# Kernel optimization log

Measured on AMD Instinct MI355X. Metric: run time of the kernel, lower is better.

The kernel has to match this reference:

```python
import jax, jax.numpy as jnp
import numpy as np

B, D, K, E = 4096, 2048, 512, 8  # tokens, model dim, kept SVD rank, experts


def setup_inputs() -> dict:
    key = jax.random.key(0)
    ks = jax.random.split(key, 7)
    x = jax.random.normal(ks[0], (B, D), dtype=jnp.float32)
    # frozen base weight (stands in for pretrained_weight)
    W = jax.random.normal(ks[1], (D, D), dtype=jnp.float32) / np.sqrt(D)
    # frozen truncated SVD factors: U_k (D,K) left vecs, V_k (K,D) as sliced in the torch code
    U_k = jnp.linalg.qr(jax.random.normal(ks[2], (D, K), dtype=jnp.float32))[0]
    V_k = jnp.linalg.qr(jax.random.normal(ks[3], (D, K), dtype=jnp.float32))[0].T
    lambda_k = jax.random.normal(ks[4], (E, K), dtype=jnp.float32) * 0.02
    v = jnp.zeros((D,), dtype=jnp.float32)
    router_W1 = jax.random.normal(ks[5], (K, 1), dtype=jnp.float32)
    router_W2 = jax.random.normal(ks[6], (1, E), dtype=jnp.float32)
    return {"x": x, "W": W, "U_k": U_k, "V_k": V_k, "lambda_k": lambda_k,
            "v": v, "router_W1": router_W1, "router_W2": router_W2}


def reference(x, W, U_k, V_k, lambda_k, v, router_W1, router_W2):
    # routing: x @ U_k -> rank-1 router -> softmax over experts
    routing = x @ U_k                                   # (B,K)
    g = jax.nn.softmax((routing @ router_W1) @ router_W2, axis=-1)  # (B,E)
    # per-expert low-rank delta weight, materialized as in the original
    delta_W = jnp.einsum('dk,ek,kn->edn', U_k, lambda_k, V_k)       # (E,D,D)
    W_tot = W[None] + delta_W                           # (E,D,D)
    # F.linear semantics: out = x @ W_tot^T per expert
    expert_out = jnp.einsum('bd,end->ben', x, W_tot)    # (B,E,D)
    out = jnp.einsum('ben,be->bn', expert_out, g)       # gated combine
    return out * (1.0 + v)
```

## Files before the change

### kernel.cpp

```cpp
#include <hip/hip_runtime.h>
#include <hip/hip_bf16.h>
#include <cstdint>

#define B_TOK 4096
#define DDIM  2048
#define KR    512
#define NE    8

using f32x4  = __attribute__((ext_vector_type(4))) float;
using short8 = __attribute__((ext_vector_type(8))) short;
using u16 = unsigned short;

__device__ inline u16 f2bf(float f) {
    union { float f; uint32_t u; } x; x.f = f;
    uint32_t u = x.u;
    return (u16)((u + 0x7fffu + ((u >> 16) & 1u)) >> 16);
}
__device__ inline float bf2f(u16 h) {
    union { uint32_t u; float f; } x; x.u = ((uint32_t)h) << 16;
    return x.f;
}

__device__ inline void gload_lds16(const u16* g, u16* l) {
    __builtin_amdgcn_global_load_lds(
        (const __attribute__((address_space(1))) void*)g,
        (__attribute__((address_space(3))) void*)l, 16, 0, 0);
}

template<int COLS4, int SRC_LD, int DST_LD>
__device__ inline void cvt_region(const float* __restrict__ src,
                                  u16* __restrict__ dst, int i) {
    int r = i / COLS4, c = i - r * COLS4;
    float4 val = *((const float4*)(src + (size_t)r * SRC_LD) + c);
    ushort4 o;
    o.x = f2bf(val.x); o.y = f2bf(val.y); o.z = f2bf(val.z); o.w = f2bf(val.w);
    *(ushort4*)(dst + (size_t)r * DST_LD + c * 4) = o;
}

__global__ __launch_bounds__(256)
void prep_all(const float* __restrict__ x, const float* __restrict__ U,
              const float* __restrict__ V, const float* __restrict__ W1,
              u16* __restrict__ Aaug, u16* __restrict__ Vb) {
    constexpr int NB_COPY = 1024;
    constexpr int N_X = 4096 * 512;
    constexpr int N_V = 512 * 512;
    constexpr int N_Z = 63 * 512;
    constexpr int N_TOT = N_X + N_V + N_Z;
    int b = blockIdx.x;
    if (b < NB_COPY) {
        for (int i = b * 256 + threadIdx.x; i < N_TOT; i += NB_COPY * 256) {
            if (i < N_X)            cvt_region<512, 2048, 2560>(x, Aaug, i);
            else if (i < N_X + N_V) cvt_region<512, 2048, 2048>(V, Vb, i - N_X);
            else {
                int z = i - (N_X + N_V);
                ushort4 zz; zz.x = 0; zz.y = 0; zz.z = 0; zz.w = 0;
                *(ushort4*)(Vb + (size_t)513 * 2048 + (size_t)z * 4) = zz;
            }
        }
    } else {
        int wrow = (b - NB_COPY) * 4 + (threadIdx.x >> 6);
        int lane = threadIdx.x & 63;
        const float* row = U + (size_t)wrow * KR;
        float s = 0.f;
        #pragma unroll
        for (int k = 0; k < KR; k += 64) s += row[k + lane] * W1[k + lane];
        #pragma unroll
        for (int o = 32; o > 0; o >>= 1) s += __shfl_down(s, o);
        if (lane == 0) Vb[(size_t)512 * 2048 + wrow] = f2bf(s);
    }
}

__global__ __launch_bounds__(256)
void router3(const u16* __restrict__ tb, const float* __restrict__ W2,
             const float* __restrict__ lam, u16* __restrict__ Am) {
    const int row = blockIdx.x * 8 + (threadIdx.x >> 5);
    const int lr = threadIdx.x & 31;
    const u16* tr = tb + (size_t)row * 576;
    float s = bf2f(tr[512]);

    float g[NE]; float mx = -1e30f;
    #pragma unroll
    for (int e = 0; e < NE; e++) { g[e] = s * W2[e]; mx = fmaxf(mx, g[e]); }
    float den = 0.f;
    #pragma unroll
    for (int e = 0; e < NE; e++) { g[e] = expf(g[e] - mx); den += g[e]; }
    float inv = 1.0f / den;

    #pragma unroll
    for (int h = 0; h < 2; h++) {
        int k = (lr + h * 32) * 8;
        short8 tv = *(const short8*)(tr + k);
        short8 ov;
        #pragma unroll
        for (int j = 0; j < 8; j++) {
            float mu = 0.f;
            #pragma unroll
            for (int e = 0; e < NE; e++) mu += g[e] * lam[e * KR + k + j];
            ov[j] = (short)f2bf(mu * inv * bf2f((u16)tv[j]));
        }
        *(short8*)(Am + (size_t)row * 2560 + 2048 + k) = ov;
    }
}

template<int BM, int BN, int WGM, int WGN, int NCOMP, bool OUT_BF16>
__global__ __launch_bounds__(256, 2)
void gemm_db(const u16* __restrict__ A, const u16* __restrict__ Bm,
             void* __restrict__ Cv,
             const float* __restrict__ Wsrc, const float* __restrict__ Usrc,
             u16* __restrict__ BigB,
             int N, int Kc, int lda, int ldb, int nbx) {
    constexpr int MF = BM / (WGM * 16);
    constexpr int NF = BN / (WGN * 16);
    constexpr int ISSA = BM / 32;
    constexpr int ISSB = BN / 32;
    __shared__ u16 sA[2 * BM * 64];
    __shared__ u16 sB[2 * BN * 64];

    if (blockIdx.x >= NCOMP) {
        constexpr int N_W = 2048 * 512;
        constexpr int N_U = 2048 * 128;
        int cb = blockIdx.x - NCOMP;
        for (int i = cb * 256 + threadIdx.x; i < N_W + N_U; i += 256 * 256) {
            if (i < N_W) cvt_region<512, 2048, 2560>(Wsrc, BigB, i);
            else         cvt_region<128, 512, 2560>(Usrc, BigB + 2048, i - N_W);
        }
        return;
    }

    const int tid = threadIdx.x;
    const int wid = tid >> 6, lane = tid & 63;
    const int l15 = lane & 15, l4 = lane >> 4;
    const int wm = wid / WGN, wn = wid % WGN;

    const int id = ((int)blockIdx.x & 7) * (NCOMP >> 3) + ((int)blockIdx.x >> 3);
    const int row0 = (id / nbx) * BM;
    const int col0 = (id % nbx) * BN;

    const int srow = tid >> 3;
    const int scol = ((tid & 7) ^ (srow & 7)) << 3;
    const u16* gA = A + (size_t)(row0 + srow) * lda + scol;
    const u16* gB = Bm + (size_t)(col0 + srow) * ldb + scol;

    f32x4 acc[MF][NF] = {};
    const int nt = Kc >> 6;

    #pragma unroll
    for (int i = 0; i < ISSA; i++)
        gload_lds16(gA + (size_t)i * 32 * lda, sA + i * 2048 + wid * 512);
    #pragma unroll
    for (int i = 0; i < ISSB; i++)
        gload_lds16(gB + (size_t)i * 32 * ldb, sB + i * 2048 + wid * 512);
    __syncthreads();

    for (int t = 0; t < nt; ++t) {
        const int cur = t & 1;
        if (t + 1 < nt) {
            const int nxt = cur ^ 1;
            const u16* gAk = gA + (size_t)(t + 1) * 64;
            const u16* gBk = gB + (size_t)(t + 1) * 64;
            #pragma unroll
            for (int i = 0; i < ISSA; i++)
                gload_lds16(gAk + (size_t)i * 32 * lda,
                            sA + nxt * BM * 64 + i * 2048 + wid * 512);
            #pragma unroll
            for (int i = 0; i < ISSB; i++)
                gload_lds16(gBk + (size_t)i * 32 * ldb,
                            sB + nxt * BN * 64 + i * 2048 + wid * 512);
        }
        const u16* a0 = sA + cur * BM * 64;
        const u16* b0 = sB + cur * BN * 64;
        #pragma unroll
        for (int kc = 0; kc < 8; kc += 4) {
            short8 af[MF], bv[NF];
            #pragma unroll
            for (int mf = 0; mf < MF; mf++) {
                int row = wm * MF * 16 + mf * 16 + l15;
                int ch = (kc + l4) ^ (row & 7);
                af[mf] = *(const short8*)(a0 + row * 64 + ch * 8);
            }
            #pragma unroll
            for (int nf = 0; nf < NF; nf++) {
                int row = wn * NF * 16 + nf * 16 + l15;
                int ch = (kc + l4) ^ (row & 7);
                bv[nf] = *(const short8*)(b0 + row * 64 + ch * 8);
            }
            #pragma unroll
            for (int mf = 0; mf < MF; mf++)
                #pragma unroll
                for (int nf = 0; nf < NF; nf++)
                    acc[mf][nf] = __builtin_amdgcn_mfma_f32_16x16x32_bf16(
                        af[mf], bv[nf], acc[mf][nf], 0, 0, 0);
        }
        __syncthreads();
    }

    #pragma unroll
    for (int nf = 0; nf < NF; nf++) {
        int col = col0 + wn * NF * 16 + nf * 16 + l15;
        #pragma unroll
        for (int mf = 0; mf < MF; mf++) {
            int row = row0 + wm * MF * 16 + mf * 16 + l4 * 4;
            #pragma unroll
            for (int r2 = 0; r2 < 4; r2++) {
                float val = acc[mf][nf][r2];
                if constexpr (OUT_BF16)
                    ((u16*)Cv)[(size_t)(row + r2) * N + col] = f2bf(val);
                else
                    ((float*)Cv)[(size_t)(row + r2) * N + col] = val;
            }
        }
    }
}

template<bool HAS_V>
__global__ __launch_bounds__(512, 1)
void gemm_ring(const u16* __restrict__ A, const u16* __restrict__ Bm,
               float* __restrict__ C, const float* __restrict__ v,
               int N, int Kc, int lda, int ldb) {
    constexpr int BM = 256, BN = 128, WGN = 2;
    constexpr int MF = 4, NF = 4;
    constexpr int SLOT = (BM + BN) * 64;
    constexpr int ROWS = 64;
    constexpr int ISSA = 4, ISSB = 2;
    __shared__ u16 lds[3 * SLOT];

    const int tid = threadIdx.x;
    const int wid = tid >> 6, lane = tid & 63;
    const int l15 = lane & 15, l4 = lane >> 4;
    const int wm = wid / WGN, wn = wid % WGN;

    const int xcd = blockIdx.x & 7;
    const int j = blockIdx.x >> 3;
    const int row0 = ((xcd >> 1) * 4 + (j >> 3)) * BM;
    const int col0 = ((xcd & 1) * 8 + (j & 7)) * BN;

    const int srow = tid >> 3;
    const int scol = ((tid & 7) ^ (srow & 7)) << 3;
    const u16* gA = A + (size_t)(row0 + srow) * lda + scol;
    const u16* gB = Bm + (size_t)(col0 + srow) * ldb + scol;

    int aoff[2][MF], boff[2][NF];
    #pragma unroll
    for (int kc = 0; kc < 2; kc++) {
        #pragma unroll
        for (int mf = 0; mf < MF; mf++) {
            int row = wm * MF * 16 + mf * 16 + l15;
            aoff[kc][mf] = row * 64 + (((kc * 4) + l4) ^ (row & 7)) * 8;
        }
        #pragma unroll
        for (int nf = 0; nf < NF; nf++) {
            int row = wn * NF * 16 + nf * 16 + l15;
            boff[kc][nf] = BM * 64 + row * 64 + (((kc * 4) + l4) ^ (row & 7)) * 8;
        }
    }

    f32x4 acc[MF][NF] = {};
    const int nt = Kc >> 6;

    #pragma unroll
    for (int p = 0; p < 2; p++) {
        const u16* gAt = gA + p * 64;
        const u16* gBt = gB + p * 64;
        u16* sl = lds + p * SLOT;
        #pragma unroll
        for (int i = 0; i < ISSA; i++)
            gload_lds16(gAt + (size_t)i * ROWS * lda,
                        sl + i * ROWS * 64 + wid * 512);
        #pragma unroll
        for (int i = 0; i < ISSB; i++)
            gload_lds16(gBt + (size_t)i * ROWS * ldb,
                        sl + BM * 64 + i * ROWS * 64 + wid * 512);
    }
    asm volatile("s_waitcnt vmcnt(6)" ::: "memory");
    __builtin_amdgcn_s_barrier();
    asm volatile("" ::: "memory");

    int sc = 0, sp = 2;
    for (int t = 0; t < nt; ++t) {
        if (t + 2 < nt) {
            const u16* gAt = gA + (size_t)(t + 2) * 64;
            const u16* gBt = gB + (size_t)(t + 2) * 64;
            u16* sl = lds + sp * SLOT;
            #pragma unroll
            for (int i = 0; i < ISSA; i++)
                gload_lds16(gAt + (size_t)i * ROWS * lda,
                            sl + i * ROWS * 64 + wid * 512);
            #pragma unroll
            for (int i = 0; i < ISSB; i++)
                gload_lds16(gBt + (size_t)i * ROWS * ldb,
                            sl + BM * 64 + i * ROWS * 64 + wid * 512);
        }
        const u16* s0 = lds + sc * SLOT;
        __builtin_amdgcn_s_setprio(1);
        #pragma unroll
        for (int kc = 0; kc < 2; kc++) {
            short8 af[MF], bv[NF];
            #pragma unroll
            for (int mf = 0; mf < MF; mf++)
                af[mf] = *(const short8*)(s0 + aoff[kc][mf]);
            #pragma unroll
            for (int nf = 0; nf < NF; nf++)
                bv[nf] = *(const short8*)(s0 + boff[kc][nf]);
            #pragma unroll
            for (int mf = 0; mf < MF; mf++)
                #pragma unroll
                for (int nf = 0; nf < NF; nf++)
                    acc[mf][nf] = __builtin_amdgcn_mfma_f32_16x16x32_bf16(
                        af[mf], bv[nf], acc[mf][nf], 0, 0, 0);
        }
        __builtin_amdgcn_s_setprio(0);

        const int rem = nt - 1 - t;
        if (rem == 0) break;
        if (rem >= 2) asm volatile("s_waitcnt vmcnt(6)" ::: "memory");
        else          asm volatile("s_waitcnt vmcnt(0)" ::: "memory");
        __builtin_amdgcn_s_barrier();
        asm volatile("" ::: "memory");
        sc = (sc == 2) ? 0 : sc + 1;
        sp = (sp == 2) ? 0 : sp + 1;
    }

    #pragma unroll
    for (int nf = 0; nf < NF; nf++) {
        int col = col0 + wn * NF * 16 + nf * 16 + l15;
        float sc2 = HAS_V ? (1.0f + v[col]) : 1.0f;
        #pragma unroll
        for (int mf = 0; mf < MF; mf++) {
            int row = row0 + wm * MF * 16 + mf * 16 + l4 * 4;
            #pragma unroll
            for (int r2 = 0; r2 < 4; r2++)
                C[(size_t)(row + r2) * N + col] = acc[mf][nf][r2] * sc2;
        }
    }
}

extern "C" void kernel_launch(void* const* d_in, const int* in_sizes, int n_in,
                              void* d_out, int out_size, void* d_ws, size_t ws_size,
                              hipStream_t stream) {
    const float* x   = (const float*)d_in[0];
    const float* W   = (const float*)d_in[1];
    const float* U   = (const float*)d_in[2];
    const float* V   = (const float*)d_in[3];
    const float* lam = (const float*)d_in[4];
    const float* v   = (const float*)d_in[5];
    const float* W1  = (const float*)d_in[6];
    const float* W2  = (const float*)d_in[7];
    float* out = (float*)d_out;

    char* ws = (char*)d_ws;
    u16* Aaug  = (u16*)ws;
    u16* BigB  = (u16*)(ws + 20971520);
    u16* Vb    = (u16*)(ws + 31457280);
    u16* tmatb = (u16*)(ws + 33816576);

    prep_all<<<1536, 256, 0, stream>>>(x, U, V, W1, Aaug, Vb);

    gemm_db<128, 64, 4, 1, 288, true><<<544, 256, 0, stream>>>(
        Aaug, Vb, tmatb, W, U, BigB, 576, 2048, 2560, 2048, 9);

    router3<<<512, 256, 0, stream>>>(tmatb, W2, lam, Aaug);

    gemm_ring<true><<<256, 512, 0, stream>>>(
        Aaug, BigB, out, v, 2048, 2560, 2560, 2560);
}
```

Before: 91.63 us.

## Read fp32 x directly in first GEMM and move x conversion into its side blocks

The first GEMM now stages fp32 x tiles into LDS with a swizzled layout and converts them to bf16 in registers before the MFMA, so it no longer waits on a separate prep pass that converted x. The x-to-bf16 conversion for the final GEMM's A operand moves into the extra copy blocks of the first GEMM, running alongside the W and U conversion, and the prep kernel shrinks to only V, zero padding and the router vector. This shortens the critical path ahead of the first GEMM, at the cost of twice the LDS and global traffic for the A tile, extra conversion ALU work in the inner loop, and fewer copy blocks (224) now handling more data.

After: 97.56 us. 6.5% more time.

```diff
diff --git a/kernel.cpp b/kernel.cpp
--- a/kernel.cpp
+++ b/kernel.cpp
@@ -19,6 +19,10 @@
 __device__ inline float bf2f(u16 h) {
     union { uint32_t u; float f; } x; x.u = ((uint32_t)h) << 16;
     return x.f;
+}
+__device__ inline short bfs(float f) {
+    __hip_bfloat16 h = __float2bfloat16(f);
+    return *reinterpret_cast<short*>(&h);
 }
 
 __device__ inline void gload_lds16(const u16* g, u16* l) {
@@ -38,21 +42,17 @@
 }
 
 __global__ __launch_bounds__(256)
-void prep_all(const float* __restrict__ x, const float* __restrict__ U,
-              const float* __restrict__ V, const float* __restrict__ W1,
-              u16* __restrict__ Aaug, u16* __restrict__ Vb) {
-    constexpr int NB_COPY = 1024;
-    constexpr int N_X = 4096 * 512;
+void prep_small(const float* __restrict__ U, const float* __restrict__ V,
+                const float* __restrict__ W1, u16* __restrict__ Vb) {
+    constexpr int NB_COPY = 64;
     constexpr int N_V = 512 * 512;
     constexpr int N_Z = 63 * 512;
-    constexpr int N_TOT = N_X + N_V + N_Z;
     int b = blockIdx.x;
     if (b < NB_COPY) {
-        for (int i = b * 256 + threadIdx.x; i < N_TOT; i += NB_COPY * 256) {
-            if (i < N_X)            cvt_region<512, 2048, 2560>(x, Aaug, i);
-            else if (i < N_X + N_V) cvt_region<512, 2048, 2048>(V, Vb, i - N_X);
+        for (int i = b * 256 + threadIdx.x; i < N_V + N_Z; i += NB_COPY * 256) {
+            if (i < N_V) cvt_region<512, 2048, 2048>(V, Vb, i);
             else {
-                int z = i - (N_X + N_V);
+                int z = i - N_V;
                 ushort4 zz; zz.x = 0; zz.y = 0; zz.z = 0; zz.w = 0;
                 *(ushort4*)(Vb + (size_t)513 * 2048 + (size_t)z * 4) = zz;
             }
@@ -102,27 +102,27 @@
     }
 }
 
-template<int BM, int BN, int WGM, int WGN, int NCOMP, bool OUT_BF16>
+template<int NCOMP>
 __global__ __launch_bounds__(256, 2)
-void gemm_db(const u16* __restrict__ A, const u16* __restrict__ Bm,
-             void* __restrict__ Cv,
-             const float* __restrict__ Wsrc, const float* __restrict__ Usrc,
-             u16* __restrict__ BigB,
-             int N, int Kc, int lda, int ldb, int nbx) {
-    constexpr int MF = BM / (WGM * 16);
-    constexpr int NF = BN / (WGN * 16);
-    constexpr int ISSA = BM / 32;
-    constexpr int ISSB = BN / 32;
-    __shared__ u16 sA[2 * BM * 64];
-    __shared__ u16 sB[2 * BN * 64];
+void gemm1_f32(const float* __restrict__ xf, const u16* __restrict__ Bm,
+               u16* __restrict__ Cb,
+               const float* __restrict__ Wsrc, const float* __restrict__ Usrc,
+               u16* __restrict__ BigB, u16* __restrict__ Aaug,
+               int N, int Kc, int nbx) {
+    constexpr int BM = 128, BN = 64;
+    constexpr int MF = 2, NF = 4;
+    __shared__ float sAf[2 * BM * 64];
+    __shared__ u16   sB [2 * BN * 64];
 
     if (blockIdx.x >= NCOMP) {
+        constexpr int N_X = 4096 * 512;
         constexpr int N_W = 2048 * 512;
         constexpr int N_U = 2048 * 128;
         int cb = blockIdx.x - NCOMP;
-        for (int i = cb * 256 + threadIdx.x; i < N_W + N_U; i += 256 * 256) {
-            if (i < N_W) cvt_region<512, 2048, 2560>(Wsrc, BigB, i);
-            else         cvt_region<128, 512, 2560>(Usrc, BigB + 2048, i - N_W);
+        for (int i = cb * 256 + threadIdx.x; i < N_X + N_W + N_U; i += 224 * 256) {
+            if (i < N_X)            cvt_region<512, 2048, 2560>(xf, Aaug, i);
+            else if (i < N_X + N_W) cvt_region<512, 2048, 2560>(Wsrc, BigB, i - N_X);
+            else                    cvt_region<128, 512, 2560>(Usrc, BigB + 2048, i - N_X - N_W);
         }
         return;
     }
@@ -130,57 +130,68 @@
     const int tid = threadIdx.x;
     const int wid = tid >> 6, lane = tid & 63;
     const int l15 = lane & 15, l4 = lane >> 4;
-    const int wm = wid / WGN, wn = wid % WGN;
+    const int wm = wid;
 
     const int id = ((int)blockIdx.x & 7) * (NCOMP >> 3) + ((int)blockIdx.x >> 3);
     const int row0 = (id / nbx) * BM;
     const int col0 = (id % nbx) * BN;
 
-    const int srow = tid >> 3;
-    const int scol = ((tid & 7) ^ (srow & 7)) << 3;
-    const u16* gA = A + (size_t)(row0 + srow) * lda + scol;
-    const u16* gB = Bm + (size_t)(col0 + srow) * ldb + scol;
+    const int sra = tid >> 4;
+    const int sca = ((tid & 15) ^ sra) << 2;
+    const float* gA = xf + (size_t)(row0 + sra) * 2048 + sca;
+    const int srb = tid >> 3;
+    const int scb = ((tid & 7) ^ (srb & 7)) << 3;
+    const u16* gB = Bm + (size_t)(col0 + srb) * 2048 + scb;
+
+    auto stageA = [&](int kt, int buf) {
+        #pragma unroll
+        for (int i = 0; i < 8; i++)
+            gload_lds16((const u16*)(gA + (size_t)i * 16 * 2048 + kt),
+                        (u16*)(sAf + buf * 8192 + i * 1024 + wid * 256));
+    };
+    auto stageB = [&](int kt, int buf) {
+        #pragma unroll
+        for (int i = 0; i < 2; i++)
+            gload_lds16(gB + (size_t)i * 32 * 2048 + kt,
+                        sB + buf * 4096 + i * 2048 + wid * 512);
+    };
 
     f32x4 acc[MF][NF] = {};
     const int nt = Kc >> 6;
 
-    #pragma unroll
-    for (int i = 0; i < ISSA; i++)
-        gload_lds16(gA + (size_t)i * 32 * lda, sA + i * 2048 + wid * 512);
-    #pragma unroll
-    for (int i = 0; i < ISSB; i++)
-        gload_lds16(gB + (size_t)i * 32 * ldb, sB + i * 2048 + wid * 512);
+    stageB(0, 0);
+    stageA(0, 0);
     __syncthreads();
 
     for (int t = 0; t < nt; ++t) {
         const int cur = t & 1;
         if (t + 1 < nt) {
-            const int nxt = cur ^ 1;
-            const u16* gAk = gA + (size_t)(t + 1) * 64;
-            const u16* gBk = gB + (size_t)(t + 1) * 64;
-            #pragma unroll
-            for (int i = 0; i < ISSA; i++)
-                gload_lds16(gAk + (size_t)i * 32 * lda,
-                            sA + nxt * BM * 64 + i * 2048 + wid * 512);
-            #pragma unroll
-            for (int i = 0; i < ISSB; i++)
-                gload_lds16(gBk + (size_t)i * 32 * ldb,
-                            sB + nxt * BN * 64 + i * 2048 + wid * 512);
-        }
-        const u16* a0 = sA + cur * BM * 64;
-        const u16* b0 = sB + cur * BN * 64;
+            stageB((t + 1) * 64, cur ^ 1);
+            stageA((t + 1) * 64, cur ^ 1);
+        }
+        const float* a0 = sAf + cur * 8192;
+        const u16*   b0 = sB + cur * 4096;
         #pragma unroll
         for (int kc = 0; kc < 8; kc += 4) {
             short8 af[MF], bv[NF];
             #pragma unroll
             for (int mf = 0; mf < MF; mf++) {
-                int row = wm * MF * 16 + mf * 16 + l15;
-                int ch = (kc + l4) ^ (row & 7);
-                af[mf] = *(const short8*)(a0 + row * 64 + ch * 8);
+                int row = wm * 32 + mf * 16 + l15;
+                int g = kc + l4;
+                int c0 = (2 * g) ^ l15;
+                int c1 = (2 * g + 1) ^ l15;
+                f32x4 p0 = *(const f32x4*)(a0 + row * 64 + c0 * 4);
+                f32x4 p1 = *(const f32x4*)(a0 + row * 64 + c1 * 4);
+                short8 h;
+                h[0] = bfs(p0[0]); h[1] = bfs(p0[1]);
+                h[2] = bfs(p0[2]); h[3] = bfs(p0[3]);
+                h[4] = bfs(p1[0]); h[5] = bfs(p1[1]);
+                h[6] = bfs(p1[2]); h[7] = bfs(p1[3]);
+                af[mf] = h;
             }
             #pragma unroll
             for (int nf = 0; nf < NF; nf++) {
-                int row = wn * NF * 16 + nf * 16 + l15;
+                int row = nf * 16 + l15;
                 int ch = (kc + l4) ^ (row & 7);
                 bv[nf] = *(const short8*)(b0 + row * 64 + ch * 8);
             }
@@ -196,18 +207,13 @@
 
     #pragma unroll
     for (int nf = 0; nf < NF; nf++) {
-        int col = col0 + wn * NF * 16 + nf * 16 + l15;
+        int col = col0 + nf * 16 + l15;
         #pragma unroll
         for (int mf = 0; mf < MF; mf++) {
-            int row = row0 + wm * MF * 16 + mf * 16 + l4 * 4;
-            #pragma unroll
-            for (int r2 = 0; r2 < 4; r2++) {
-                float val = acc[mf][nf][r2];
-                if constexpr (OUT_BF16)
-                    ((u16*)Cv)[(size_t)(row + r2) * N + col] = f2bf(val);
-                else
-                    ((float*)Cv)[(size_t)(row + r2) * N + col] = val;
-            }
+            int row = row0 + wm * 32 + mf * 16 + l4 * 4;
+            #pragma unroll
+            for (int r2 = 0; r2 < 4; r2++)
+                Cb[(size_t)(row + r2) * N + col] = f2bf(acc[mf][nf][r2]);
         }
     }
 }
@@ -353,10 +359,10 @@
     u16* Vb    = (u16*)(ws + 31457280);
     u16* tmatb = (u16*)(ws + 33816576);
 
-    prep_all<<<1536, 256, 0, stream>>>(x, U, V, W1, Aaug, Vb);
-
-    gemm_db<128, 64, 4, 1, 288, true><<<544, 256, 0, stream>>>(
-        Aaug, Vb, tmatb, W, U, BigB, 576, 2048, 2560, 2048, 9);
+    prep_small<<<576, 256, 0, stream>>>(U, V, W1, Vb);
+
+    gemm1_f32<288><<<512, 256, 0, stream>>>(
+        x, Vb, tmatb, W, U, BigB, Aaug, 576, 2048, 9);
 
     router3<<<512, 256, 0, stream>>>(tmatb, W2, lam, Aaug);
 
```
